# Performance work log

Measured on AMD Instinct MI355X. Metric: run time of the kernel, lower is better.

Reference implementation:

```python
import jax, jax.numpy as jnp
import numpy as np

K = 20  # max object ids (ids 1..K); masks value 0 = background
EPS_GN = 1e-5

def _conv3(x, w, b):
    # 3x3 conv, padding=1 == SAME, NCHW/OIHW
    y = jax.lax.conv_general_dilated(x, w, (1, 1), 'SAME',
                                     dimension_numbers=('NCHW', 'OIHW', 'NCHW'))
    return y + b[None, :, None, None]

def _groupnorm(x, groups, w, b):
    B, C, H, W = x.shape
    xg = x.reshape(B, groups, C // groups, H, W)
    m = xg.mean(axis=(2, 3, 4), keepdims=True)
    v = xg.var(axis=(2, 3, 4), keepdims=True)
    xn = ((xg - m) * jax.lax.rsqrt(v + EPS_GN)).reshape(B, C, H, W)
    return xn * w[None, :, None, None] + b[None, :, None, None]


def setup_inputs() -> dict:
    key = jax.random.key(0)
    ks = jax.random.split(key, 8)
    def p(k, shape, s=0.05):
        return jax.random.normal(k, shape, jnp.float32) * s
    return {
        'x': jax.random.normal(ks[0], (4, 512, 128, 128), jnp.float32),
        'masks': jax.random.randint(ks[1], (4, 128, 128), 0, 21, jnp.int32),
        'w1': p(ks[2], (256, 512, 3, 3)), 'b1': jnp.zeros((256,), jnp.float32),
        'g1w': jnp.ones((256,), jnp.float32), 'g1b': jnp.zeros((256,), jnp.float32),
        'w2': p(ks[3], (128, 256, 3, 3)), 'b2': jnp.zeros((128,), jnp.float32),
        'g2w': jnp.ones((128,), jnp.float32), 'g2b': jnp.zeros((128,), jnp.float32),
        'w3': p(ks[4], (64, 128, 3, 3)), 'b3': jnp.zeros((64,), jnp.float32),
        'g3w': jnp.ones((64,), jnp.float32), 'g3b': jnp.zeros((64,), jnp.float32),
        'wb': p(ks[5], (7, 64)), 'bb': jnp.zeros((7,), jnp.float32),
        'wc': p(ks[6], (1, 64)), 'bc': jnp.zeros((1,), jnp.float32),
    }


def reference(x, masks, w1, b1, g1w, g1b, w2, b2, g2w, g2b,
              w3, b3, g3w, g3b, wb, bb, wc, bc):
    # encoder: (conv3 -> GN -> relu) x3
    h = jax.nn.relu(_groupnorm(_conv3(x, w1, b1), 8, g1w, g1b))
    h = jax.nn.relu(_groupnorm(_conv3(h, w2, b2), 4, g2w, g2b))
    h = jax.nn.relu(_groupnorm(_conv3(h, w3, b3), 4, g3w, g3b))  # [B,64,H,W]

    # masked segment-mean pooling over all ids 1..K (vectorized unique-loop)
    ids = jnp.arange(1, K + 1, dtype=masks.dtype)
    onehot = (masks[:, None, :, :] == ids[None, :, None, None]).astype(h.dtype)  # [B,K,H,W]
    sums = jnp.einsum('bchw,bkhw->bkc', h, onehot)          # [B,K,64]
    counts = onehot.sum(axis=(2, 3))                        # [B,K]
    pooled = sums / (counts[..., None] + 1e-6)              # [B,K,64]

    # 1x1 conv heads on pooled vector == dense matmuls
    boxes = jnp.einsum('bkc,oc->bko', pooled, wb) + bb      # [B,K,7]
    scores = jax.nn.sigmoid(jnp.einsum('bkc,oc->bko', pooled, wc) + bc)[..., 0]  # [B,K]
    return (boxes, scores)
```

## Files before the change

kernel.cpp:

```cpp
#include <hip/hip_runtime.h>
#include <hip/hip_bf16.h>
#include <math.h>

#define HW 16384
#define BATCH 4
#define KIDS 20

using short8 = __attribute__((ext_vector_type(8))) short;
using f32x4  = __attribute__((ext_vector_type(4))) float;

__device__ __forceinline__ unsigned short bfbits(float f) {
  __hip_bfloat16 h = __float2bfloat16(f);
  return *(unsigned short*)&h;
}

__device__ __forceinline__ void gload_lds16(const void* g, void* l) {
  __builtin_amdgcn_global_load_lds(
      (const __attribute__((address_space(1))) void*)g,
      (__attribute__((address_space(3))) void*)l, 16, 0, 0);
}

__global__ __launch_bounds__(256) void zero_k(float* __restrict__ p, int n) {
  int i = blockIdx.x*256 + threadIdx.x;
  if (i < n) p[i] = 0.f;
}

__global__ __launch_bounds__(256) void x_to_nhwc_k(const float* __restrict__ in,
                                                   __hip_bfloat16* __restrict__ out)
{
  __shared__ float tile[32][65];
  int t = blockIdx.x;
  const int pxt = t & 255; t >>= 8;
  const int ct  = t & 15;  t >>= 4;
  const int b   = t;
  const int tid = threadIdx.x;
  #pragma unroll
  for (int it = 0; it < 8; ++it) {
    int idx = tid + it*256;
    int px_l = idx & 63, c_l = idx >> 6;
    tile[c_l][px_l] = in[((size_t)(b*512 + ct*32 + c_l))*HW + pxt*64 + px_l];
  }
  __syncthreads();
  #pragma unroll
  for (int it = 0; it < 4; ++it) {
    int idx = tid + it*256;
    int c2 = idx & 15, px_l = idx >> 4;
    unsigned u = ((unsigned)bfbits(tile[c2*2+1][px_l]) << 16) | bfbits(tile[c2*2][px_l]);
    *(unsigned*)(out + ((size_t)(b*HW + pxt*64 + px_l))*512 + ct*32 + c2*2) = u;
  }
}

template<int Co, int Ci>
__global__ __launch_bounds__(256) void pack_w_k(const float* __restrict__ w,
                                                __hip_bfloat16* __restrict__ out)
{
  const int i = blockIdx.x*256 + threadIdx.x;
  const int ci = i & (Ci-1);
  const int r  = i >> __builtin_ctz(Ci);
  const int co = r & (Co-1);
  const int t  = r >> __builtin_ctz(Co);
  out[i] = __float2bfloat16(w[((size_t)co*Ci + ci)*9 + t]);
}

template<int Ci, int Co, int ROWS, int CPG, int MT>
__global__ __launch_bounds__(512, 2) void conv_mfma_k(
    const __hip_bfloat16* __restrict__ xin,
    const __hip_bfloat16* __restrict__ wpk,
    const float* __restrict__ bias,
    float* __restrict__ out,
    float* __restrict__ partS, float* __restrict__ partSS)
{
  constexpr int PXW = (8/ROWS)/2;
  constexpr int WN  = 128/PXW;
  constexpr int NT  = WN/16;
  constexpr int SR  = ROWS + 2;
  constexpr int RG  = 128 / ROWS;
  constexpr int NC  = Ci / 32;
  constexpr int NGW = (MT*16)/CPG;
  constexpr int BSZ = SR*130*32;
  __shared__ __align__(16) short bl[2*BSZ];

  const int b  = blockIdx.x / RG;
  const int r0 = (blockIdx.x % RG) * ROWS;
  const int co0 = blockIdx.y * (2*MT*16);
  const int tid = threadIdx.x;
  const int wave = tid >> 6, lane = tid & 63;
  const int row_w = wave % ROWS;
  const int rem   = wave / ROWS;
  const int pw    = rem % PXW;
  const int coh   = rem / PXW;
  const int co_w  = co0 + coh*MT*16;
  const int y = r0 + row_w;
  const int lr = lane & 15, q = lane >> 4;
  const int px_s = lane >> 2, q16_s = lane & 3;

  if (tid < 2*SR*2*4) {
    int u = tid; int q16 = u & 3; u >>= 2;
    int side = u & 1; u >>= 1;
    int r = u % SR, buf = u / SR;
    short8 z = {0,0,0,0,0,0,0,0};
    *(short8*)(bl + buf*BSZ + (r*130 + (side ? 129 : 0))*32 + q16*8) = z;
  }
  if (r0 == 0) {
    short8 z = {0,0,0,0,0,0,0,0};
    for (int i = tid; i < 2*520; i += 512) {
      int buf = i / 520, j = i % 520;
      *((short8*)(bl + buf*BSZ) + j) = z;
    }
  }
  if (r0 == 128-ROWS) {
    short8 z = {0,0,0,0,0,0,0,0};
    for (int i = tid; i < 2*520; i += 512) {
      int buf = i / 520, j = i % 520;
      *((short8*)(bl + buf*BSZ + (SR-1)*130*32) + j) = z;
    }
  }

  const size_t in_base = (size_t)b * HW * Ci;
  auto stage = [&](int buf, int ci0) {
    #pragma unroll
    for (int it = 0; it < SR; ++it) {
      int gi = wave*SR + it;
      int r = gi >> 3, seg = gi & 7;
      int yy = r0 + r - 1;
      if ((unsigned)yy < 128u) {
        const __hip_bfloat16* src = xin + in_base
            + (size_t)(yy*128 + seg*16 + px_s)*Ci + ci0 + q16_s*8;
        gload_lds16(src, bl + buf*BSZ + (r*130 + seg*16 + 1)*32);
      }
    }
  };

  f32x4 acc[MT][NT] = {};
  stage(0, 0);
  __syncthreads();
  int cur = 0;
  for (int c = 0; c < NC; ++c) {
    const int ci0 = c*32;
    if (c+1 < NC) stage(cur^1, ci0 + 32);
    const short* blc = bl + cur*BSZ;
    short8 wreg[2][MT];
    #pragma unroll
    for (int mt = 0; mt < MT; ++mt)
      wreg[0][mt] = *(const short8*)(wpk +
          ((size_t)(0*Co + co_w + mt*16 + lr))*Ci + ci0 + q*8);
    #pragma unroll
    for (int t = 0; t < 9; ++t) {
      const int cb = t & 1, nb = cb ^ 1;
      if (t < 8) {
        #pragma unroll
        for (int mt = 0; mt < MT; ++mt)
          wreg[nb][mt] = *(const short8*)(wpk +
              ((size_t)((t+1)*Co + co_w + mt*16 + lr))*Ci + ci0 + q*8);
      }
      const int dy = t / 3, dx = t % 3;
      short8 bf[NT];
      #pragma unroll
      for (int nt = 0; nt < NT; ++nt) {
        int px = pw*WN + nt*16 + lr;
        bf[nt] = *(const short8*)(blc + ((row_w + dy)*130 + px + dx)*32 + q*8);
      }
      #pragma unroll
      for (int mt = 0; mt < MT; ++mt)
        #pragma unroll
        for (int nt = 0; nt < NT; ++nt)
          acc[mt][nt] = __builtin_amdgcn_mfma_f32_16x16x32_bf16(
              wreg[cb][mt], bf[nt], acc[mt][nt], 0, 0, 0);
    }
    __syncthreads();
    cur ^= 1;
  }

  float sg[NGW] = {}, ssg[NGW] = {};
  #pragma unroll
  for (int mt = 0; mt < MT; ++mt) {
    const int g = (mt*16) / CPG;
    #pragma unroll
    for (int nt = 0; nt < NT; ++nt) {
      int px = pw*WN + nt*16 + lr;
      int co = co_w + mt*16 + q*4;
      const float4 bv = *(const float4*)(bias + co);
      f32x4 v = acc[mt][nt];
      v[0] += bv.x; v[1] += bv.y; v[2] += bv.z; v[3] += bv.w;
      sg[g]  += v[0] + v[1] + v[2] + v[3];
      ssg[g] += v[0]*v[0] + v[1]*v[1] + v[2]*v[2] + v[3]*v[3];
      *(f32x4*)(out + ((size_t)(b*HW + y*128 + px))*Co + co) = v;
    }
  }
  const int bgbase = b*(Co/CPG) + co_w/CPG;
  #pragma unroll
  for (int g = 0; g < NGW; ++g) {
    float s = sg[g], ss = ssg[g];
    #pragma unroll
    for (int off = 32; off; off >>= 1) {
      s  += __shfl_xor(s, off);
      ss += __shfl_xor(ss, off);
    }
    if (lane == 0) {
      atomicAdd(&partS[bgbase + g], s);
      atomicAdd(&partSS[bgbase + g], ss);
    }
  }
}

__global__ void gn_final_k(const float* __restrict__ partS,
                           const float* __restrict__ partSS,
                           float* __restrict__ mv, int nbg, float inv_n)
{
  const int i = threadIdx.x;
  if (i < nbg) {
    float s = partS[i], ss = partSS[i];
    float mean = s*inv_n, var = ss*inv_n - mean*mean;
    mv[2*i] = mean; mv[2*i+1] = rsqrtf(var + 1e-5f);
  }
}

template<int C, int CPG, bool BF16OUT>
__global__ __launch_bounds__(256) void gn_apply_k(const float* __restrict__ in,
    const float* __restrict__ mv, const float* __restrict__ gw,
    const float* __restrict__ gb, void* __restrict__ outp)
{
  constexpr int C4 = C/4;
  constexpr int G = C/CPG;
  const int i = blockIdx.x*256 + threadIdx.x;
  const int c4 = i & (C4-1);
  const int pxb = i >> __builtin_ctz(C4);
  const int b = pxb >> 14;
  const int c = c4*4;
  const int bg = b*G + c/CPG;
  const float mean = mv[2*bg], inv = mv[2*bg+1];
  float4 v = *((const float4*)in + i);
  const float4 w4 = *(const float4*)(gw + c);
  const float4 b4 = *(const float4*)(gb + c);
  float r0 = fmaxf((v.x-mean)*inv*w4.x + b4.x, 0.f);
  float r1 = fmaxf((v.y-mean)*inv*w4.y + b4.y, 0.f);
  float r2 = fmaxf((v.z-mean)*inv*w4.z + b4.z, 0.f);
  float r3 = fmaxf((v.w-mean)*inv*w4.w + b4.w, 0.f);
  if (BF16OUT) {
    uint2 o;
    o.x = ((unsigned)bfbits(r1) << 16) | bfbits(r0);
    o.y = ((unsigned)bfbits(r3) << 16) | bfbits(r2);
    *(uint2*)((__hip_bfloat16*)outp + (size_t)i*4) = o;
  } else {
    *((float4*)outp + i) = make_float4(r0,r1,r2,r3);
  }
}

__global__ __launch_bounds__(256) void pool_counts_k(
    const int* __restrict__ masks, float* __restrict__ counts)
{
  __shared__ int hist[KIDS];
  const int b = blockIdx.x;
  if (threadIdx.x < KIDS) hist[threadIdx.x] = 0;
  __syncthreads();
  for (int p = threadIdx.x; p < HW; p += 256) {
    const int m = masks[b*HW + p];
    if (m > 0) atomicAdd(&hist[m-1], 1);
  }
  __syncthreads();
  if (threadIdx.x < KIDS) counts[b*KIDS + threadIdx.x] = (float)hist[threadIdx.x];
}

__global__ __launch_bounds__(256) void pool_sums_k(const float* __restrict__ h3,
    const int* __restrict__ masks, float* __restrict__ sums)
{
  __shared__ float acc[KIDS*64];
  const int b = blockIdx.x >> 5, chunk = blockIdx.x & 31;
  const int tid = threadIdx.x;
  for (int j = tid; j < KIDS*64; j += 256) acc[j] = 0.f;
  __syncthreads();
  const int ch = tid & 63, pi = tid >> 6;
  const int p0 = chunk*512;
  for (int p = p0 + pi; p < p0 + 512; p += 4) {
    int m = masks[b*HW + p];
    if (m > 0) atomicAdd(&acc[(m-1)*64 + ch], h3[((size_t)(b*HW + p))*64 + ch]);
  }
  __syncthreads();
  for (int j = tid; j < KIDS*64; j += 256) atomicAdd(&sums[b*KIDS*64 + j], acc[j]);
}

__global__ __launch_bounds__(64) void heads_k(
    const float* __restrict__ sums, const float* __restrict__ counts,
    const float* __restrict__ wb, const float* __restrict__ bb,
    const float* __restrict__ wc, const float* __restrict__ bc,
    float* __restrict__ out)
{
  const int bk = blockIdx.x;
  const int c = threadIdx.x;
  const float pooled = sums[bk*64 + c] / (counts[bk] + 1e-6f);
  #pragma unroll
  for (int o = 0; o < 7; ++o) {
    float t = pooled * wb[o*64 + c];
    for (int off = 32; off > 0; off >>= 1) t += __shfl_down(t, off);
    if (c == 0) out[bk*7 + o] = t + bb[o];
  }
  float t = pooled * wc[c];
  for (int off = 32; off > 0; off >>= 1) t += __shfl_down(t, off);
  if (c == 0) out[BATCH*KIDS*7 + bk] = 1.f / (1.f + expf(-(t + bc[0])));
}

extern "C" void kernel_launch(void* const* d_in, const int* in_sizes, int n_in,
                              void* d_out, int out_size, void* d_ws, size_t ws_size,
                              hipStream_t stream)
{
  const float* x     = (const float*)d_in[0];
  const int*   masks = (const int*)  d_in[1];
  const float* w1 = (const float*)d_in[2];
  const float* b1 = (const float*)d_in[3];
  const float* g1w= (const float*)d_in[4];
  const float* g1b= (const float*)d_in[5];
  const float* w2 = (const float*)d_in[6];
  const float* b2 = (const float*)d_in[7];
  const float* g2w= (const float*)d_in[8];
  const float* g2b= (const float*)d_in[9];
  const float* w3 = (const float*)d_in[10];
  const float* b3 = (const float*)d_in[11];
  const float* g3w= (const float*)d_in[12];
  const float* g3b= (const float*)d_in[13];
  const float* wb = (const float*)d_in[14];
  const float* bb = (const float*)d_in[15];
  const float* wc = (const float*)d_in[16];
  const float* bc = (const float*)d_in[17];
  float* out = (float*)d_out;

  char* ws = (char*)d_ws;
  __hip_bfloat16* xb  = (__hip_bfloat16*)ws;
  __hip_bfloat16* h1b = (__hip_bfloat16*)ws;
  __hip_bfloat16* h2b = (__hip_bfloat16*)(ws + (size_t)(32<<20));
  float*          h3  = (float*)         (ws + (size_t)(48<<20));
  float* c1 = (float*)(ws + (size_t)(64<<20));
  float* c2 = c1;
  float* c3 = (float*)(ws + (size_t)(96<<20));
  __hip_bfloat16* wp1 = (__hip_bfloat16*)(ws + (size_t)(128<<20));
  __hip_bfloat16* wp2 = wp1 + 9*256*512;
  __hip_bfloat16* wp3 = wp2 + 9*128*256;
  char* tail = (char*)(wp3 + 9*64*128);
  float* mv     = (float*)tail;
  float* partS  = mv + 64;
  float* partSS = partS + 64;
  float* sums   = partSS + 64;
  float* counts = sums + 5120;

  zero_k<<<21, 256, 0, stream>>>(partS, 64 + 64 + 5120);

  x_to_nhwc_k<<<16384, 256, 0, stream>>>(x, xb);
  pack_w_k<256,512><<<4608, 256, 0, stream>>>(w1, wp1);
  pack_w_k<128,256><<<1152, 256, 0, stream>>>(w2, wp2);
  pack_w_k< 64,128><<< 288, 256, 0, stream>>>(w3, wp3);

  conv_mfma_k<512,256,4,32,4><<<dim3(128,2), 512, 0, stream>>>(
      xb, wp1, b1, c1, partS, partSS);
  gn_final_k<<<1, 64, 0, stream>>>(partS, partSS, mv, 32, 1.f/(32.f*HW));
  gn_apply_k<256,32,true><<<16384, 256, 0, stream>>>(c1, mv, g1w, g1b, h1b);

  conv_mfma_k<256,128,2,32,4><<<dim3(256,1), 512, 0, stream>>>(
      h1b, wp2, b2, c2, partS + 32, partSS + 32);
  gn_final_k<<<1, 64, 0, stream>>>(partS + 32, partSS + 32, mv, 16, 1.f/(32.f*HW));
  gn_apply_k<128,32,true><<<8192, 256, 0, stream>>>(c2, mv, g2w, g2b, h2b);

  conv_mfma_k<128,64,2,16,2><<<dim3(256,1), 512, 0, stream>>>(
      h2b, wp3, b3, c3, partS + 48, partSS + 48);
  gn_final_k<<<1, 64, 0, stream>>>(partS + 48, partSS + 48, mv, 16, 1.f/(16.f*HW));
  gn_apply_k<64,16,false><<<4096, 256, 0, stream>>>(c3, mv, g3w, g3b, h3);

  pool_counts_k<<<BATCH, 256, 0, stream>>>(masks, counts);
  pool_sums_k<<<BATCH*32, 256, 0, stream>>>(h3, masks, sums);
  heads_k<<<BATCH*KIDS, 64, 0, stream>>>(sums, counts, wb, bb, wc, bc, out);
}
```

Before: 798.1 us.

## Stage conv weights in LDS via async loads and fix two-row tiling

The conv kernel now copies the per-chunk weight slice for all nine taps into shared memory with global_load_lds, and waves read A fragments from LDS. Before, each wave fetched its weights straight from global memory into registers. Sync moves to explicit vmcnt waits and raw s_barrier. Conv1 also changes from four rows per block to two rows per block, which doubles its grid. This adds LDS footprint and weight-staging traffic on every chunk, and the handwritten vmcnt counts must match the number of loads issued or the kernel can race.

```diff
diff --git a/kernel.cpp b/kernel.cpp
--- a/kernel.cpp
+++ b/kernel.cpp
@@ -62,7 +62,7 @@
   out[i] = __float2bfloat16(w[((size_t)co*Ci + ci)*9 + t]);
 }
 
-template<int Ci, int Co, int ROWS, int CPG, int MT>
+template<int Ci, int Co, int CPG, int MT>
 __global__ __launch_bounds__(512, 2) void conv_mfma_k(
     const __hip_bfloat16* __restrict__ xin,
     const __hip_bfloat16* __restrict__ wpk,
@@ -70,104 +70,103 @@
     float* __restrict__ out,
     float* __restrict__ partS, float* __restrict__ partSS)
 {
-  constexpr int PXW = (8/ROWS)/2;
-  constexpr int WN  = 128/PXW;
-  constexpr int NT  = WN/16;
-  constexpr int SR  = ROWS + 2;
-  constexpr int RG  = 128 / ROWS;
-  constexpr int NC  = Ci / 32;
+  constexpr int ROWS = 2, NT = 4, SR = 4, RG = 64;
+  constexpr int WCO = 2*MT*16;
+  constexpr int NC  = Ci/32;
   constexpr int NGW = (MT*16)/CPG;
-  constexpr int BSZ = SR*130*32;
-  __shared__ __align__(16) short bl[2*BSZ];
+  constexpr int IB  = SR*130*32;
+  constexpr int UW  = 9*WCO/16;
+  __shared__ __align__(16) short lds[2*IB + 9*WCO*32];
+  short* const wlds = lds + 2*IB;
 
   const int b  = blockIdx.x / RG;
   const int r0 = (blockIdx.x % RG) * ROWS;
-  const int co0 = blockIdx.y * (2*MT*16);
+  const int co0 = blockIdx.y * WCO;
   const int tid = threadIdx.x;
   const int wave = tid >> 6, lane = tid & 63;
-  const int row_w = wave % ROWS;
-  const int rem   = wave / ROWS;
-  const int pw    = rem % PXW;
-  const int coh   = rem / PXW;
+  const int row_w = wave & 1;
+  const int pw    = (wave >> 1) & 1;
+  const int coh   = wave >> 2;
   const int co_w  = co0 + coh*MT*16;
   const int y = r0 + row_w;
   const int lr = lane & 15, q = lane >> 4;
-  const int px_s = lane >> 2, q16_s = lane & 3;
-
-  if (tid < 2*SR*2*4) {
-    int u = tid; int q16 = u & 3; u >>= 2;
-    int side = u & 1; u >>= 1;
-    int r = u % SR, buf = u / SR;
+  const int ls = lane >> 2, lq = lane & 3;
+
+  if (tid < 64) {
+    int q16 = tid & 3, u = tid >> 2;
+    int side = u & 1, r = (u >> 1) & 3, buf = u >> 3;
     short8 z = {0,0,0,0,0,0,0,0};
-    *(short8*)(bl + buf*BSZ + (r*130 + (side ? 129 : 0))*32 + q16*8) = z;
+    *(short8*)(lds + buf*IB + (r*130 + (side ? 129 : 0))*32 + q16*8) = z;
   }
   if (r0 == 0) {
     short8 z = {0,0,0,0,0,0,0,0};
     for (int i = tid; i < 2*520; i += 512) {
       int buf = i / 520, j = i % 520;
-      *((short8*)(bl + buf*BSZ) + j) = z;
-    }
-  }
-  if (r0 == 128-ROWS) {
+      *((short8*)(lds + buf*IB) + j) = z;
+    }
+  }
+  if (r0 == 126) {
     short8 z = {0,0,0,0,0,0,0,0};
     for (int i = tid; i < 2*520; i += 512) {
       int buf = i / 520, j = i % 520;
-      *((short8*)(bl + buf*BSZ + (SR-1)*130*32) + j) = z;
+      *((short8*)(lds + buf*IB + (SR-1)*130*32) + j) = z;
     }
   }
 
   const size_t in_base = (size_t)b * HW * Ci;
-  auto stage = [&](int buf, int ci0) {
+  auto stage_i = [&](int buf, int ci0) {
     #pragma unroll
-    for (int it = 0; it < SR; ++it) {
-      int gi = wave*SR + it;
+    for (int it = 0; it < 4; ++it) {
+      int gi = wave*4 + it;
       int r = gi >> 3, seg = gi & 7;
       int yy = r0 + r - 1;
-      if ((unsigned)yy < 128u) {
-        const __hip_bfloat16* src = xin + in_base
-            + (size_t)(yy*128 + seg*16 + px_s)*Ci + ci0 + q16_s*8;
-        gload_lds16(src, bl + buf*BSZ + (r*130 + seg*16 + 1)*32);
-      }
+      if ((unsigned)yy < 128u)
+        gload_lds16(xin + in_base + (size_t)(yy*128 + seg*16 + ls)*Ci + ci0 + lq*8,
+                    lds + buf*IB + (r*130 + seg*16 + 1)*32);
     }
   };
+  auto stage_w = [&](int ci0) {
+    for (int u = wave; u < UW; u += 8) {
+      int t = u / (WCO/16), cb = u % (WCO/16);
+      gload_lds16(wpk + ((size_t)(t*Co + co0 + cb*16 + ls))*Ci + ci0 + lq*8,
+                  wlds + (t*WCO + cb*16)*32);
+    }
+  };
 
   f32x4 acc[MT][NT] = {};
-  stage(0, 0);
+  stage_i(0, 0);
   __syncthreads();
   int cur = 0;
   for (int c = 0; c < NC; ++c) {
     const int ci0 = c*32;
-    if (c+1 < NC) stage(cur^1, ci0 + 32);
-    const short* blc = bl + cur*BSZ;
-    short8 wreg[2][MT];
-    #pragma unroll
-    for (int mt = 0; mt < MT; ++mt)
-      wreg[0][mt] = *(const short8*)(wpk +
-          ((size_t)(0*Co + co_w + mt*16 + lr))*Ci + ci0 + q*8);
+    stage_w(ci0);
+    if (c+1 < NC) {
+      stage_i(cur^1, ci0 + 32);
+      asm volatile("s_waitcnt vmcnt(4)" ::: "memory");
+    } else {
+      asm volatile("s_waitcnt vmcnt(0)" ::: "memory");
+    }
+    __builtin_amdgcn_s_barrier();
+    __builtin_amdgcn_sched_barrier(0);
+    const short* ib = lds + cur*IB;
     #pragma unroll
     for (int t = 0; t < 9; ++t) {
-      const int cb = t & 1, nb = cb ^ 1;
-      if (t < 8) {
-        #pragma unroll
-        for (int mt = 0; mt < MT; ++mt)
-          wreg[nb][mt] = *(const short8*)(wpk +
-              ((size_t)((t+1)*Co + co_w + mt*16 + lr))*Ci + ci0 + q*8);
-      }
-      const int dy = t / 3, dx = t % 3;
-      short8 bf[NT];
+      const int dy = t/3, dx = t%3;
+      short8 af[MT], bf[NT];
       #pragma unroll
-      for (int nt = 0; nt < NT; ++nt) {
-        int px = pw*WN + nt*16 + lr;
-        bf[nt] = *(const short8*)(blc + ((row_w + dy)*130 + px + dx)*32 + q*8);
-      }
+      for (int mt = 0; mt < MT; ++mt)
+        af[mt] = *(const short8*)(wlds + (t*WCO + coh*MT*16 + mt*16 + lr)*32 + q*8);
+      #pragma unroll
+      for (int nt = 0; nt < NT; ++nt)
+        bf[nt] = *(const short8*)(ib + ((row_w+dy)*130 + pw*64 + nt*16 + lr + dx)*32 + q*8);
       #pragma unroll
       for (int mt = 0; mt < MT; ++mt)
         #pragma unroll
         for (int nt = 0; nt < NT; ++nt)
           acc[mt][nt] = __builtin_amdgcn_mfma_f32_16x16x32_bf16(
-              wreg[cb][mt], bf[nt], acc[mt][nt], 0, 0, 0);
-    }
-    __syncthreads();
+              af[mt], bf[nt], acc[mt][nt], 0, 0, 0);
+    }
+    __builtin_amdgcn_s_barrier();
     cur ^= 1;
   }
 
@@ -177,7 +176,7 @@
     const int g = (mt*16) / CPG;
     #pragma unroll
     for (int nt = 0; nt < NT; ++nt) {
-      int px = pw*WN + nt*16 + lr;
+      int px = pw*64 + nt*16 + lr;
       int co = co_w + mt*16 + q*4;
       const float4 bv = *(const float4*)(bias + co);
       f32x4 v = acc[mt][nt];
@@ -348,17 +347,17 @@
   pack_w_k<128,256><<<1152, 256, 0, stream>>>(w2, wp2);
   pack_w_k< 64,128><<< 288, 256, 0, stream>>>(w3, wp3);
 
-  conv_mfma_k<512,256,4,32,4><<<dim3(128,2), 512, 0, stream>>>(
+  conv_mfma_k<512,256,32,4><<<dim3(256,2), 512, 0, stream>>>(
       xb, wp1, b1, c1, partS, partSS);
   gn_final_k<<<1, 64, 0, stream>>>(partS, partSS, mv, 32, 1.f/(32.f*HW));
   gn_apply_k<256,32,true><<<16384, 256, 0, stream>>>(c1, mv, g1w, g1b, h1b);
 
-  conv_mfma_k<256,128,2,32,4><<<dim3(256,1), 512, 0, stream>>>(
+  conv_mfma_k<256,128,32,4><<<dim3(256,1), 512, 0, stream>>>(
       h1b, wp2, b2, c2, partS + 32, partSS + 32);
   gn_final_k<<<1, 64, 0, stream>>>(partS + 32, partSS + 32, mv, 16, 1.f/(32.f*HW));
   gn_apply_k<128,32,true><<<8192, 256, 0, stream>>>(c2, mv, g2w, g2b, h2b);
 
-  conv_mfma_k<128,64,2,16,2><<<dim3(256,1), 512, 0, stream>>>(
+  conv_mfma_k<128,64,16,2><<<dim3(256,1), 512, 0, stream>>>(
       h2b, wp3, b3, c3, partS + 48, partSS + 48);
   gn_final_k<<<1, 64, 0, stream>>>(partS + 48, partSS + 48, mv, 16, 1.f/(16.f*HW));
   gn_apply_k<64,16,false><<<4096, 256, 0, stream>>>(c3, mv, g3w, g3b, h3);
```

Measured after the change: 706.0 us. 1.13x faster.
